# Kernel tuning notes

Hardware: AMD Instinct MI355X
Metric: run time of the kernel (lower is better)

The kernel has to match this reference:

```python
import jax, jax.numpy as jnp
import numpy as np

DIM = 768
NUM_HEADS = 12
HEAD_DIM = DIM // NUM_HEADS
EPS = 1e-5


def setup_inputs() -> dict:
    key = jax.random.key(0)
    ks = jax.random.split(key, 12)
    s = 0.02
    return {
        "x": jax.random.normal(ks[0], (8, 1024, DIM), jnp.float32),
        "pos_embed": jax.random.normal(ks[1], (8, 1024, DIM), jnp.float32),
        "gamma": jnp.ones((DIM,), jnp.float32),
        "beta": jnp.zeros((DIM,), jnp.float32),
        "Wq": jax.random.normal(ks[2], (DIM, DIM), jnp.float32) * s,
        "bq": jnp.zeros((DIM,), jnp.float32),
        "Wk": jax.random.normal(ks[3], (DIM, DIM), jnp.float32) * s,
        "bk": jnp.zeros((DIM,), jnp.float32),
        "Wv": jax.random.normal(ks[4], (DIM, DIM), jnp.float32) * s,
        "bv": jnp.zeros((DIM,), jnp.float32),
        "Wo": jax.random.normal(ks[5], (DIM, DIM), jnp.float32) * s,
        "bo": jnp.zeros((DIM,), jnp.float32),
    }


def _split_heads(t):
    B, N, C = t.shape
    return t.reshape(B, N, NUM_HEADS, HEAD_DIM).transpose(0, 2, 1, 3)  # (B,H,N,D)


def reference(x, pos_embed, gamma, beta, Wq, bq, Wk, bk, Wv, bv, Wo, bo):
    B, N, C = x.shape
    # pre-LayerNorm
    mu = jnp.mean(x, axis=-1, keepdims=True)
    var = jnp.mean(jnp.square(x - mu), axis=-1, keepdims=True)
    x_norm = (x - mu) * jax.lax.rsqrt(var + EPS) * gamma + beta

    Q = _split_heads(x_norm @ Wq + bq) + _split_heads(pos_embed)  # pos-embed added to Q
    K = _split_heads(x_norm @ Wk + bk)
    V = _split_heads(x_norm @ Wv + bv)

    inv_temp = 1.0 / jnp.sqrt(jnp.float32(HEAD_DIM))
    S = jnp.einsum("bhnd,bhmd->bhnm", Q, K) * inv_temp  # (B,H,N,N)
    A = jax.nn.softmax(S, axis=-1)  # dropout p=0.0 -> identity
    vals = jnp.einsum("bhnm,bhmd->bhnd", A, V)
    vals = vals.transpose(0, 2, 1, 3).reshape(B, N, C)
    return vals @ Wo + bo + x  # residual
```

## Files before the change

### kernel.cpp

```cpp
#include <hip/hip_runtime.h>
#include <hip/hip_bf16.h>

#define TOK 8192
#define CDIM 768
#define NH 12
#define HD 64
#define QKV_N 2304
#define QSCALE 0.18033688011f
#define MREF 10.0f

typedef __attribute__((ext_vector_type(8))) short bf16x8;
typedef __attribute__((ext_vector_type(4))) float f32x4;
typedef unsigned short ushort_t;

__device__ __forceinline__ ushort_t f2bf(float f) {
  unsigned u = __float_as_uint(f);
  u += 0x7fffu + ((u >> 16) & 1u);
  return (ushort_t)(u >> 16);
}

__device__ __forceinline__ f32x4 mfma16(bf16x8 a, bf16x8 b, f32x4 c) {
  return __builtin_amdgcn_mfma_f32_16x16x32_bf16(a, b, c, 0, 0, 0);
}

__device__ __forceinline__ int swz(int r) { return (r ^ (r >> 3)) & 7; }

__device__ __forceinline__ void gload16(const void* g, void* l) {
  __builtin_amdgcn_global_load_lds(
      (const __attribute__((address_space(1))) unsigned int*)g,
      (__attribute__((address_space(3))) unsigned int*)l, 16, 0, 0);
}

__global__ __launch_bounds__(256) void ln_kernel(const float* __restrict__ x,
                                                 const float* __restrict__ gamma,
                                                 const float* __restrict__ beta,
                                                 ushort_t* __restrict__ xn) {
  int t = blockIdx.x;
  const float* row = x + (size_t)t * CDIM;
  float v[3];
  float s = 0.f, s2 = 0.f;
#pragma unroll
  for (int i = 0; i < 3; i++) {
    v[i] = row[threadIdx.x + 256 * i];
    s += v[i];
    s2 += v[i] * v[i];
  }
#pragma unroll
  for (int off = 32; off; off >>= 1) {
    s += __shfl_xor(s, off);
    s2 += __shfl_xor(s2, off);
  }
  __shared__ float red[8];
  int wid = threadIdx.x >> 6, lane = threadIdx.x & 63;
  if (lane == 0) { red[wid] = s; red[wid + 4] = s2; }
  __syncthreads();
  s = red[0] + red[1] + red[2] + red[3];
  s2 = red[4] + red[5] + red[6] + red[7];
  float mu = s * (1.f / CDIM);
  float var = s2 * (1.f / CDIM) - mu * mu;
  float rstd = rsqrtf(var + 1e-5f);
  ushort_t* orow = xn + (size_t)t * CDIM;
#pragma unroll
  for (int i = 0; i < 3; i++) {
    int c = threadIdx.x + 256 * i;
    orow[c] = f2bf((v[i] - mu) * rstd * gamma[c] + beta[c]);
  }
}

__global__ __launch_bounds__(256) void wtrans_kernel(const float* __restrict__ Wq,
                                                     const float* __restrict__ Wk,
                                                     const float* __restrict__ Wv,
                                                     const float* __restrict__ Wo,
                                                     ushort_t* __restrict__ wt) {
  const float* W = (blockIdx.z == 0) ? Wq : (blockIdx.z == 1) ? Wk
                   : (blockIdx.z == 2) ? Wv : Wo;
  __shared__ float tile[32][33];
  int tr = blockIdx.y, tc = blockIdx.x;
  int tx = threadIdx.x, ty = threadIdx.y;
#pragma unroll
  for (int j = 0; j < 4; j++) {
    int k = tr * 32 + ty + j * 8;
    tile[ty + j * 8][tx] = W[(size_t)k * CDIM + tc * 32 + tx];
  }
  __syncthreads();
  ushort_t* o = wt + (size_t)blockIdx.z * CDIM * CDIM;
#pragma unroll
  for (int j = 0; j < 4; j++) {
    int n = tc * 32 + ty + j * 8;
    o[(size_t)n * CDIM + tr * 32 + tx] = f2bf(tile[tx][ty + j * 8]);
  }
}

__global__ __launch_bounds__(256) void gemm0_kernel(
    const ushort_t* __restrict__ A, const ushort_t* __restrict__ Bt,
    const float* __restrict__ bq, const float* __restrict__ bk,
    const float* __restrict__ bv, const float* __restrict__ pos,
    ushort_t* __restrict__ outp) {
  __shared__ __align__(16) ushort_t lds_a[128][40];
  __shared__ __align__(16) ushort_t lds_b[128][40];
  const int bn = blockIdx.x, bm = blockIdx.y;
  const int tid = threadIdx.x;
  const int lane = tid & 63, wid = tid >> 6;
  const int wr = wid >> 1, wc = wid & 1;
  const int l16 = lane & 15, lg = lane >> 4;
  f32x4 acc[4][4] = {};

  for (int k0 = 0; k0 < CDIM; k0 += 32) {
#pragma unroll
    for (int i = 0; i < 2; i++) {
      int ch = tid + 256 * i;
      int row = ch >> 2, c8 = (ch & 3) * 8;
      *reinterpret_cast<uint4*>(&lds_a[row][c8]) =
          *reinterpret_cast<const uint4*>(&A[(size_t)(bm * 128 + row) * CDIM + k0 + c8]);
      *reinterpret_cast<uint4*>(&lds_b[row][c8]) =
          *reinterpret_cast<const uint4*>(&Bt[(size_t)(bn * 128 + row) * CDIM + k0 + c8]);
    }
    __syncthreads();
    bf16x8 af[4], bfr[4];
#pragma unroll
    for (int mi = 0; mi < 4; mi++)
      af[mi] = *reinterpret_cast<const bf16x8*>(&lds_a[wr * 64 + mi * 16 + l16][8 * lg]);
#pragma unroll
    for (int ni = 0; ni < 4; ni++)
      bfr[ni] = *reinterpret_cast<const bf16x8*>(&lds_b[wc * 64 + ni * 16 + l16][8 * lg]);
#pragma unroll
    for (int mi = 0; mi < 4; mi++)
#pragma unroll
      for (int ni = 0; ni < 4; ni++)
        acc[mi][ni] = mfma16(af[mi], bfr[ni], acc[mi][ni]);
    __syncthreads();
  }

#pragma unroll
  for (int mi = 0; mi < 4; mi++)
#pragma unroll
    for (int ni = 0; ni < 4; ni++)
#pragma unroll
      for (int r = 0; r < 4; r++) {
        int grow = bm * 128 + wr * 64 + mi * 16 + 4 * lg + r;
        int gcol = bn * 128 + wc * 64 + ni * 16 + l16;
        float v = acc[mi][ni][r];
        if (gcol < 768) {
          v = (v + bq[gcol] + pos[(size_t)grow * CDIM + gcol]) * QSCALE;
        } else if (gcol < 1536) {
          v += bk[gcol - 768];
        } else {
          v += bv[gcol - 1536];
        }
        outp[(size_t)grow * QKV_N + gcol] = f2bf(v);
      }
}

__global__ __launch_bounds__(256) void gemm1_kernel(
    const ushort_t* __restrict__ A, const ushort_t* __restrict__ Bt,
    const float* __restrict__ b0, const float* __restrict__ extra,
    float* __restrict__ outp) {
  __shared__ __align__(16) ushort_t lds_a[2][128 * 64];
  __shared__ __align__(16) ushort_t lds_b[2][128 * 64];
  const int NB = 6;
  int lin = blockIdx.y * NB + blockIdx.x;
  int nl = (lin & 7) * (NB * 8) + (lin >> 3);
  const int bn = nl % NB, bm = nl / NB;

  const int tid = threadIdx.x;
  const int lane = tid & 63, wid = tid >> 6;
  const int wr = wid >> 1, wc = wid & 1;
  const int l16 = lane & 15, lg = lane >> 4;
  f32x4 acc[4][4] = {};

  int aoff[2][4], boff[2][4];
#pragma unroll
  for (int kk = 0; kk < 2; kk++) {
#pragma unroll
    for (int mi = 0; mi < 4; mi++) {
      int r = wr * 64 + mi * 16 + l16;
      aoff[kk][mi] = r * 64 + (((kk * 4 + lg) ^ swz(r)) & 7) * 8;
    }
#pragma unroll
    for (int ni = 0; ni < 4; ni++) {
      int r = wc * 64 + ni * 16 + l16;
      boff[kk][ni] = r * 64 + (((kk * 4 + lg) ^ swz(r)) & 7) * 8;
    }
  }

  auto stage = [&](int buf, int k0) {
#pragma unroll
    for (int i = 0; i < 4; i++) {
      int slot = i * 256 + tid;
      int row = slot >> 3, j = slot & 7;
      int c8 = ((j ^ swz(row)) & 7) * 8;
      gload16(&A[(size_t)(bm * 128 + row) * CDIM + k0 + c8], &lds_a[buf][slot * 8]);
      gload16(&Bt[(size_t)(bn * 128 + row) * CDIM + k0 + c8], &lds_b[buf][slot * 8]);
    }
  };

  stage(0, 0);
  asm volatile("s_waitcnt vmcnt(0)" ::: "memory");
  __builtin_amdgcn_s_barrier();
  __builtin_amdgcn_sched_barrier(0);

  int cur = 0;
#pragma unroll 2
  for (int t = 0; t < 12; t++) {
    if (t < 11) stage(cur ^ 1, (t + 1) * 64);
#pragma unroll
    for (int kk = 0; kk < 2; kk++) {
      bf16x8 af[4], bfr[4];
#pragma unroll
      for (int mi = 0; mi < 4; mi++)
        af[mi] = *reinterpret_cast<const bf16x8*>(&lds_a[cur][aoff[kk][mi]]);
#pragma unroll
      for (int ni = 0; ni < 4; ni++)
        bfr[ni] = *reinterpret_cast<const bf16x8*>(&lds_b[cur][boff[kk][ni]]);
      __builtin_amdgcn_s_setprio(1);
#pragma unroll
      for (int mi = 0; mi < 4; mi++)
#pragma unroll
        for (int ni = 0; ni < 4; ni++)
          acc[mi][ni] = mfma16(af[mi], bfr[ni], acc[mi][ni]);
      __builtin_amdgcn_s_setprio(0);
    }
    asm volatile("s_waitcnt vmcnt(0) lgkmcnt(0)" ::: "memory");
    __builtin_amdgcn_s_barrier();
    __builtin_amdgcn_sched_barrier(0);
    cur ^= 1;
  }

#pragma unroll
  for (int mi = 0; mi < 4; mi++)
#pragma unroll
    for (int ni = 0; ni < 4; ni++)
#pragma unroll
      for (int r = 0; r < 4; r++) {
        int grow = bm * 128 + wr * 64 + mi * 16 + 4 * lg + r;
        int gcol = bn * 128 + wc * 64 + ni * 16 + l16;
        outp[(size_t)grow * CDIM + gcol] =
            acc[mi][ni][r] + b0[gcol] + extra[(size_t)grow * CDIM + gcol];
      }
}

__global__ __launch_bounds__(256, 3) void attn_kernel(const ushort_t* __restrict__ QKV,
                                                      ushort_t* __restrict__ O) {
  const int b = blockIdx.x, h = blockIdx.y, qt = blockIdx.z;

  const int tid = threadIdx.x, lane = tid & 63, w = tid >> 6;
  const int l16 = lane & 15, lg = lane >> 4;
  const int tb = b * 1024 + qt * 128;
  const int co_q = h * HD, co_k = CDIM + h * HD, co_v = 2 * CDIM + h * HD;

  __shared__ __align__(16) ushort_t k_lds[2][64 * 64];
  __shared__ __align__(16) ushort_t vt_lds[2][64 * 64];
  __shared__ __align__(16) ushort_t p_lds[128 * 64];

  bf16x8 qf[2][2];
#pragma unroll
  for (int mi = 0; mi < 2; mi++)
#pragma unroll
    for (int ds = 0; ds < 2; ds++)
      qf[mi][ds] = *reinterpret_cast<const bf16x8*>(
          &QKV[(size_t)(tb + w * 32 + mi * 16 + l16) * QKV_N + co_q + ds * 32 + 8 * lg]);

  float m_sm[2] = {MREF, MREF};
  float l_sm[2] = {0.f, 0.f};
  float m_acc[2][4];
#pragma unroll
  for (int mi = 0; mi < 2; mi++)
#pragma unroll
    for (int r = 0; r < 4; r++) m_acc[mi][r] = MREF;
  f32x4 oacc[2][4] = {};

  int kfoff[2][4];
#pragma unroll
  for (int ds = 0; ds < 2; ds++)
#pragma unroll
    for (int ni = 0; ni < 4; ni++) {
      int rr = ni * 16 + l16;
      kfoff[ds][ni] = rr * 64 + (((ds * 4 + lg) ^ swz(rr)) & 7) * 8;
    }
  int poff[2][4], paoff[2][2];
#pragma unroll
  for (int mi = 0; mi < 2; mi++) {
    int myq = w * 32 + mi * 16 + l16;
    int sq = swz(myq);
#pragma unroll
    for (int ni = 0; ni < 4; ni++)
      poff[mi][ni] = myq * 64 + (lg & 1) * 4 + (((ni * 2 + (lg >> 1)) ^ sq) & 7) * 8;
#pragma unroll
    for (int ks = 0; ks < 2; ks++)
      paoff[mi][ks] = myq * 64 + (((ks * 4 + lg) ^ sq) & 7) * 8;
  }
  int vboff[2][4];
#pragma unroll
  for (int ks = 0; ks < 2; ks++)
#pragma unroll
    for (int ni = 0; ni < 4; ni++) {
      int d = ni * 16 + l16;
      vboff[ks][ni] = d * 64 + (((ks * 4 + lg) ^ swz(d)) & 7) * 8;
    }

  auto stage_k = [&](int buf, int kt) {
    const int kv0 = kt * 64;
#pragma unroll
    for (int i = 0; i < 2; i++) {
      int slot = i * 256 + tid;
      int r = slot >> 3, j = slot & 7;
      int c = ((j ^ swz(r)) & 7) * 8;
      gload16(&QKV[(size_t)(b * 1024 + kv0 + r) * QKV_N + co_k + c],
              &k_lds[buf][slot * 8]);
    }
  };

  const int kv0 = (tid >> 3) * 2, d0 = (tid & 7) * 8;
  const int sV = ((kv0 >> 3) ^ (d0 >> 3)) & 7;
  int voff[8];
#pragma unroll
  for (int u = 0; u < 8; u++)
    voff[u] = (d0 + u) * 64 + ((sV ^ u) & 7) * 8 + (kv0 & 7);
  const ushort_t* vsrc = QKV + (size_t)(b * 1024 + kv0) * QKV_N + co_v + d0;

  uint4 vr0, vr1;
  auto load_v = [&](int kt) {
    vr0 = *reinterpret_cast<const uint4*>(vsrc + (size_t)kt * 64 * QKV_N);
    vr1 = *reinterpret_cast<const uint4*>(vsrc + (size_t)kt * 64 * QKV_N + QKV_N);
  };
  auto write_v = [&](int buf) {
    const unsigned* w0 = reinterpret_cast<const unsigned*>(&vr0);
    const unsigned* w1 = reinterpret_cast<const unsigned*>(&vr1);
#pragma unroll
    for (int u = 0; u < 8; u++) {
      unsigned a = w0[u >> 1], c = w1[u >> 1];
      unsigned val = (u & 1) ? ((a >> 16) | (c & 0xffff0000u))
                             : ((a & 0xffffu) | (c << 16));
      *reinterpret_cast<unsigned*>(&vt_lds[buf][voff[u]]) = val;
    }
  };

  stage_k(0, 0);
  load_v(0);
  write_v(0);
  asm volatile("s_waitcnt vmcnt(0) lgkmcnt(0)" ::: "memory");
  __builtin_amdgcn_s_barrier();
  __builtin_amdgcn_sched_barrier(0);

  for (int kt = 0; kt < 16; kt++) {
    const int cur = kt & 1, nxt = cur ^ 1;
    if (kt < 15) { stage_k(nxt, kt + 1); load_v(kt + 1); }

    bf16x8 kf[2][4];
#pragma unroll
    for (int ds = 0; ds < 2; ds++)
#pragma unroll
      for (int ni = 0; ni < 4; ni++)
        kf[ds][ni] = *reinterpret_cast<const bf16x8*>(&k_lds[cur][kfoff[ds][ni]]);

#pragma unroll
    for (int mi = 0; mi < 2; mi++) {
      f32x4 st[4] = {};
      __builtin_amdgcn_s_setprio(1);
#pragma unroll
      for (int ds = 0; ds < 2; ds++)
#pragma unroll
        for (int ni = 0; ni < 4; ni++)
          st[ni] = mfma16(kf[ds][ni], qf[mi][ds], st[ni]);
      __builtin_amdgcn_s_setprio(0);

      float t0 = fmaxf(fmaxf(st[0][0], st[0][1]), fmaxf(st[0][2], st[0][3]));
      float t1 = fmaxf(fmaxf(st[1][0], st[1][1]), fmaxf(st[1][2], st[1][3]));
      float t2 = fmaxf(fmaxf(st[2][0], st[2][1]), fmaxf(st[2][2], st[2][3]));
      float t3 = fmaxf(fmaxf(st[3][0], st[3][1]), fmaxf(st[3][2], st[3][3]));
      float tm = fmaxf(fmaxf(t0, t1), fmaxf(t2, t3));

      if (__any(tm > m_sm[mi])) {
        float rm = fmaxf(tm, __shfl_xor(tm, 16));
        rm = fmaxf(rm, __shfl_xor(rm, 32));
        float mnew = fmaxf(m_sm[mi], rm);
        l_sm[mi] *= exp2f(m_sm[mi] - mnew);
        m_sm[mi] = mnew;
#pragma unroll
        for (int r = 0; r < 4; r++) {
          float mn = __shfl(mnew, 4 * lg + r);
          float corr = exp2f(m_acc[mi][r] - mn);
          m_acc[mi][r] = mn;
#pragma unroll
          for (int ni = 0; ni < 4; ni++) oacc[mi][ni][r] *= corr;
        }
      }

      float ps[4];
#pragma unroll
      for (int ni = 0; ni < 4; ni++) {
        float e0 = exp2f(st[ni][0] - m_sm[mi]);
        float e1 = exp2f(st[ni][1] - m_sm[mi]);
        float e2 = exp2f(st[ni][2] - m_sm[mi]);
        float e3 = exp2f(st[ni][3] - m_sm[mi]);
        st[ni][0] = e0; st[ni][1] = e1; st[ni][2] = e2; st[ni][3] = e3;
        ps[ni] = (e0 + e1) + (e2 + e3);
      }
      l_sm[mi] += (ps[0] + ps[1]) + (ps[2] + ps[3]);

#pragma unroll
      for (int ni = 0; ni < 4; ni++) {
        unsigned p01, p23;
        asm("v_cvt_pk_bf16_f32 %0, %1, %2" : "=v"(p01) : "v"(st[ni][0]), "v"(st[ni][1]));
        asm("v_cvt_pk_bf16_f32 %0, %1, %2" : "=v"(p23) : "v"(st[ni][2]), "v"(st[ni][3]));
        uint2 pk; pk.x = p01; pk.y = p23;
        *reinterpret_cast<uint2*>(&p_lds[poff[mi][ni]]) = pk;
      }
    }

#pragma unroll
    for (int ks = 0; ks < 2; ks++) {
      bf16x8 pa0 = *reinterpret_cast<const bf16x8*>(&p_lds[paoff[0][ks]]);
      bf16x8 pa1 = *reinterpret_cast<const bf16x8*>(&p_lds[paoff[1][ks]]);
      bf16x8 vb[4];
#pragma unroll
      for (int ni = 0; ni < 4; ni++)
        vb[ni] = *reinterpret_cast<const bf16x8*>(&vt_lds[cur][vboff[ks][ni]]);
      __builtin_amdgcn_s_setprio(1);
#pragma unroll
      for (int ni = 0; ni < 4; ni++) {
        oacc[0][ni] = mfma16(pa0, vb[ni], oacc[0][ni]);
        oacc[1][ni] = mfma16(pa1, vb[ni], oacc[1][ni]);
      }
      __builtin_amdgcn_s_setprio(0);
    }

    if (kt < 15) write_v(nxt);
    asm volatile("s_waitcnt vmcnt(0) lgkmcnt(0)" ::: "memory");
    __builtin_amdgcn_s_barrier();
    __builtin_amdgcn_sched_barrier(0);
  }

#pragma unroll
  for (int mi = 0; mi < 2; mi++) {
    float l = l_sm[mi];
    l += __shfl_xor(l, 16);
    l += __shfl_xor(l, 32);
#pragma unroll
    for (int r = 0; r < 4; r++) {
      float lr = __shfl(l, 4 * lg + r);
      float inv = 1.f / lr;
      int grow = tb + w * 32 + mi * 16 + 4 * lg + r;
#pragma unroll
      for (int ni = 0; ni < 4; ni++) {
        int gcol = h * HD + ni * 16 + l16;
        O[(size_t)grow * CDIM + gcol] = f2bf(oacc[mi][ni][r] * inv);
      }
    }
  }
}

extern "C" void kernel_launch(void* const* d_in, const int* in_sizes, int n_in,
                              void* d_out, int out_size, void* d_ws, size_t ws_size,
                              hipStream_t stream) {
  const float* x     = (const float*)d_in[0];
  const float* pos   = (const float*)d_in[1];
  const float* gamma = (const float*)d_in[2];
  const float* beta  = (const float*)d_in[3];
  const float* Wq    = (const float*)d_in[4];
  const float* bq    = (const float*)d_in[5];
  const float* Wk    = (const float*)d_in[6];
  const float* bk    = (const float*)d_in[7];
  const float* Wv    = (const float*)d_in[8];
  const float* bv    = (const float*)d_in[9];
  const float* Wo    = (const float*)d_in[10];
  const float* bo    = (const float*)d_in[11];
  float* out = (float*)d_out;

  ushort_t* xn   = (ushort_t*)d_ws;
  ushort_t* wt   = xn + (size_t)TOK * CDIM;
  ushort_t* qkv  = wt + (size_t)3072 * CDIM;
  ushort_t* aout = qkv + (size_t)TOK * QKV_N;

  ln_kernel<<<TOK, 256, 0, stream>>>(x, gamma, beta, xn);
  wtrans_kernel<<<dim3(24, 24, 4), dim3(32, 8), 0, stream>>>(Wq, Wk, Wv, Wo, wt);
  gemm0_kernel<<<dim3(18, 64), 256, 0, stream>>>(xn, wt, bq, bk, bv, pos, qkv);
  attn_kernel<<<dim3(8, NH, 8), 256, 0, stream>>>(qkv, aout);
  gemm1_kernel<<<dim3(6, 64), 256, 0, stream>>>(aout, wt + (size_t)QKV_N * CDIM,
                                                bo, x, out);
}
```

Before: 172.6 us.

## Merge LN and weight transpose into one launch; pipeline QKV GEMM with async LDS loads

```diff
diff --git a/kernel.cpp b/kernel.cpp
--- a/kernel.cpp
+++ b/kernel.cpp
@@ -31,63 +31,65 @@
       (__attribute__((address_space(3))) unsigned int*)l, 16, 0, 0);
 }
 
-__global__ __launch_bounds__(256) void ln_kernel(const float* __restrict__ x,
-                                                 const float* __restrict__ gamma,
-                                                 const float* __restrict__ beta,
-                                                 ushort_t* __restrict__ xn) {
-  int t = blockIdx.x;
-  const float* row = x + (size_t)t * CDIM;
-  float v[3];
-  float s = 0.f, s2 = 0.f;
-#pragma unroll
-  for (int i = 0; i < 3; i++) {
-    v[i] = row[threadIdx.x + 256 * i];
-    s += v[i];
-    s2 += v[i] * v[i];
-  }
-#pragma unroll
-  for (int off = 32; off; off >>= 1) {
-    s += __shfl_xor(s, off);
-    s2 += __shfl_xor(s2, off);
-  }
+__global__ __launch_bounds__(256) void prep_kernel(
+    const float* __restrict__ x, const float* __restrict__ gamma,
+    const float* __restrict__ beta, ushort_t* __restrict__ xn,
+    const float* __restrict__ Wq, const float* __restrict__ Wk,
+    const float* __restrict__ Wv, const float* __restrict__ Wo,
+    ushort_t* __restrict__ wt) {
   __shared__ float red[8];
-  int wid = threadIdx.x >> 6, lane = threadIdx.x & 63;
-  if (lane == 0) { red[wid] = s; red[wid + 4] = s2; }
-  __syncthreads();
-  s = red[0] + red[1] + red[2] + red[3];
-  s2 = red[4] + red[5] + red[6] + red[7];
-  float mu = s * (1.f / CDIM);
-  float var = s2 * (1.f / CDIM) - mu * mu;
-  float rstd = rsqrtf(var + 1e-5f);
-  ushort_t* orow = xn + (size_t)t * CDIM;
-#pragma unroll
-  for (int i = 0; i < 3; i++) {
-    int c = threadIdx.x + 256 * i;
-    orow[c] = f2bf((v[i] - mu) * rstd * gamma[c] + beta[c]);
-  }
-}
-
-__global__ __launch_bounds__(256) void wtrans_kernel(const float* __restrict__ Wq,
-                                                     const float* __restrict__ Wk,
-                                                     const float* __restrict__ Wv,
-                                                     const float* __restrict__ Wo,
-                                                     ushort_t* __restrict__ wt) {
-  const float* W = (blockIdx.z == 0) ? Wq : (blockIdx.z == 1) ? Wk
-                   : (blockIdx.z == 2) ? Wv : Wo;
   __shared__ float tile[32][33];
-  int tr = blockIdx.y, tc = blockIdx.x;
-  int tx = threadIdx.x, ty = threadIdx.y;
-#pragma unroll
-  for (int j = 0; j < 4; j++) {
-    int k = tr * 32 + ty + j * 8;
-    tile[ty + j * 8][tx] = W[(size_t)k * CDIM + tc * 32 + tx];
-  }
-  __syncthreads();
-  ushort_t* o = wt + (size_t)blockIdx.z * CDIM * CDIM;
-#pragma unroll
-  for (int j = 0; j < 4; j++) {
-    int n = tc * 32 + ty + j * 8;
-    o[(size_t)n * CDIM + tr * 32 + tx] = f2bf(tile[tx][ty + j * 8]);
+  const int bid = blockIdx.x;
+  const int tid = threadIdx.x;
+
+  if (bid < TOK) {
+    const float* row = x + (size_t)bid * CDIM;
+    float v[3];
+    float s = 0.f, s2 = 0.f;
+#pragma unroll
+    for (int i = 0; i < 3; i++) {
+      v[i] = row[tid + 256 * i];
+      s += v[i];
+      s2 += v[i] * v[i];
+    }
+#pragma unroll
+    for (int off = 32; off; off >>= 1) {
+      s += __shfl_xor(s, off);
+      s2 += __shfl_xor(s2, off);
+    }
+    int wid = tid >> 6, lane = tid & 63;
+    if (lane == 0) { red[wid] = s; red[wid + 4] = s2; }
+    __syncthreads();
+    s = red[0] + red[1] + red[2] + red[3];
+    s2 = red[4] + red[5] + red[6] + red[7];
+    float mu = s * (1.f / CDIM);
+    float var = s2 * (1.f / CDIM) - mu * mu;
+    float rstd = rsqrtf(var + 1e-5f);
+    ushort_t* orow = xn + (size_t)bid * CDIM;
+#pragma unroll
+    for (int i = 0; i < 3; i++) {
+      int c = tid + 256 * i;
+      orow[c] = f2bf((v[i] - mu) * rstd * gamma[c] + beta[c]);
+    }
+  } else {
+    int zi = bid - TOK;
+    int z = zi / 576;
+    int rem = zi % 576;
+    int trr = rem / 24, tcc = rem % 24;
+    const float* W = (z == 0) ? Wq : (z == 1) ? Wk : (z == 2) ? Wv : Wo;
+    int tx = tid & 31, ty = tid >> 5;
+#pragma unroll
+    for (int j = 0; j < 4; j++) {
+      int k = trr * 32 + ty + j * 8;
+      tile[ty + j * 8][tx] = W[(size_t)k * CDIM + tcc * 32 + tx];
+    }
+    __syncthreads();
+    ushort_t* o = wt + (size_t)z * CDIM * CDIM;
+#pragma unroll
+    for (int j = 0; j < 4; j++) {
+      int n = tcc * 32 + ty + j * 8;
+      o[(size_t)n * CDIM + trr * 32 + tx] = f2bf(tile[tx][ty + j * 8]);
+    }
   }
 }
 
@@ -96,39 +98,75 @@
     const float* __restrict__ bq, const float* __restrict__ bk,
     const float* __restrict__ bv, const float* __restrict__ pos,
     ushort_t* __restrict__ outp) {
-  __shared__ __align__(16) ushort_t lds_a[128][40];
-  __shared__ __align__(16) ushort_t lds_b[128][40];
-  const int bn = blockIdx.x, bm = blockIdx.y;
+  __shared__ __align__(16) ushort_t lds_a[2][128 * 64];
+  __shared__ __align__(16) ushort_t lds_b[2][128 * 64];
+  const int NB = 18;
+  int lin = blockIdx.y * NB + blockIdx.x;
+  int nl = (lin & 7) * (NB * 8) + (lin >> 3);
+  const int bn = nl % NB, bm = nl / NB;
+
   const int tid = threadIdx.x;
   const int lane = tid & 63, wid = tid >> 6;
   const int wr = wid >> 1, wc = wid & 1;
   const int l16 = lane & 15, lg = lane >> 4;
   f32x4 acc[4][4] = {};
 
-  for (int k0 = 0; k0 < CDIM; k0 += 32) {
-#pragma unroll
-    for (int i = 0; i < 2; i++) {
-      int ch = tid + 256 * i;
-      int row = ch >> 2, c8 = (ch & 3) * 8;
-      *reinterpret_cast<uint4*>(&lds_a[row][c8]) =
-          *reinterpret_cast<const uint4*>(&A[(size_t)(bm * 128 + row) * CDIM + k0 + c8]);
-      *reinterpret_cast<uint4*>(&lds_b[row][c8]) =
-          *reinterpret_cast<const uint4*>(&Bt[(size_t)(bn * 128 + row) * CDIM + k0 + c8]);
-    }
-    __syncthreads();
-    bf16x8 af[4], bfr[4];
-#pragma unroll
-    for (int mi = 0; mi < 4; mi++)
-      af[mi] = *reinterpret_cast<const bf16x8*>(&lds_a[wr * 64 + mi * 16 + l16][8 * lg]);
-#pragma unroll
-    for (int ni = 0; ni < 4; ni++)
-      bfr[ni] = *reinterpret_cast<const bf16x8*>(&lds_b[wc * 64 + ni * 16 + l16][8 * lg]);
-#pragma unroll
-    for (int mi = 0; mi < 4; mi++)
+  int aoff[2][4], boff[2][4];
+#pragma unroll
+  for (int kk = 0; kk < 2; kk++) {
+#pragma unroll
+    for (int mi = 0; mi < 4; mi++) {
+      int r = wr * 64 + mi * 16 + l16;
+      aoff[kk][mi] = r * 64 + (((kk * 4 + lg) ^ swz(r)) & 7) * 8;
+    }
+#pragma unroll
+    for (int ni = 0; ni < 4; ni++) {
+      int r = wc * 64 + ni * 16 + l16;
+      boff[kk][ni] = r * 64 + (((kk * 4 + lg) ^ swz(r)) & 7) * 8;
+    }
+  }
+
+  auto stage = [&](int buf, int k0) {
+#pragma unroll
+    for (int i = 0; i < 4; i++) {
+      int slot = i * 256 + tid;
+      int row = slot >> 3, j = slot & 7;
+      int c8 = ((j ^ swz(row)) & 7) * 8;
+      gload16(&A[(size_t)(bm * 128 + row) * CDIM + k0 + c8], &lds_a[buf][slot * 8]);
+      gload16(&Bt[(size_t)(bn * 128 + row) * CDIM + k0 + c8], &lds_b[buf][slot * 8]);
+    }
+  };
+
+  stage(0, 0);
+  asm volatile("s_waitcnt vmcnt(0)" ::: "memory");
+  __builtin_amdgcn_s_barrier();
+  __builtin_amdgcn_sched_barrier(0);
+
+  int cur = 0;
+#pragma unroll 2
+  for (int t = 0; t < 12; t++) {
+    if (t < 11) stage(cur ^ 1, (t + 1) * 64);
+#pragma unroll
+    for (int kk = 0; kk < 2; kk++) {
+      bf16x8 af[4], bfr[4];
+#pragma unroll
+      for (int mi = 0; mi < 4; mi++)
+        af[mi] = *reinterpret_cast<const bf16x8*>(&lds_a[cur][aoff[kk][mi]]);
 #pragma unroll
       for (int ni = 0; ni < 4; ni++)
-        acc[mi][ni] = mfma16(af[mi], bfr[ni], acc[mi][ni]);
-    __syncthreads();
+        bfr[ni] = *reinterpret_cast<const bf16x8*>(&lds_b[cur][boff[kk][ni]]);
+      __builtin_amdgcn_s_setprio(1);
+#pragma unroll
+      for (int mi = 0; mi < 4; mi++)
+#pragma unroll
+        for (int ni = 0; ni < 4; ni++)
+          acc[mi][ni] = mfma16(af[mi], bfr[ni], acc[mi][ni]);
+      __builtin_amdgcn_s_setprio(0);
+    }
+    asm volatile("s_waitcnt vmcnt(0) lgkmcnt(0)" ::: "memory");
+    __builtin_amdgcn_s_barrier();
+    __builtin_amdgcn_sched_barrier(0);
+    cur ^= 1;
   }
 
 #pragma unroll
@@ -472,8 +510,8 @@
   ushort_t* qkv  = wt + (size_t)3072 * CDIM;
   ushort_t* aout = qkv + (size_t)TOK * QKV_N;
 
-  ln_kernel<<<TOK, 256, 0, stream>>>(x, gamma, beta, xn);
-  wtrans_kernel<<<dim3(24, 24, 4), dim3(32, 8), 0, stream>>>(Wq, Wk, Wv, Wo, wt);
+  prep_kernel<<<TOK + 2304, 256, 0, stream>>>(x, gamma, beta, xn,
+                                              Wq, Wk, Wv, Wo, wt);
   gemm0_kernel<<<dim3(18, 64), 256, 0, stream>>>(xn, wt, bq, bk, bv, pos, qkv);
   attn_kernel<<<dim3(8, NH, 8), 256, 0, stream>>>(qkv, aout);
   gemm1_kernel<<<dim3(6, 64), 256, 0, stream>>>(aout, wt + (size_t)QKV_N * CDIM,
```

New measurement: 165.9 us. -3.9%, faster.
